# Kernel tuning notes

Measured on AMD Instinct MI355X. Metric: run time of the kernel, lower is better.

## Reference

```python
import jax, jax.numpy as jnp
import numpy as np

N, E, G, F_IN, H, C = 50000, 800000, 512, 128, 96, 10
BN_EPS = 1e-5


def _bn(x, w, b):
    # torch BatchNorm1d training-mode forward: batch stats, biased variance
    mu = jnp.mean(x, axis=0)
    var = jnp.var(x, axis=0)
    return (x - mu) * jax.lax.rsqrt(var + BN_EPS) * w + b


def setup_inputs() -> dict:
    key = jax.random.key(0)
    ks = iter(jax.random.split(key, 64))

    def rn(shape, s=0.05):
        return jax.random.normal(next(ks), shape, jnp.float32) * s

    inp = {
        "x": jax.random.normal(next(ks), (N, F_IN), jnp.float32),
        "edge_index": jax.random.randint(next(ks), (2, E), 0, N, dtype=jnp.int32),
        "batch": jnp.sort(jax.random.randint(next(ks), (N,), 0, G, dtype=jnp.int32)),
        "bn_feat_w": jnp.ones((F_IN,), jnp.float32),
        "bn_feat_b": jnp.full((F_IN,), 1e-4, jnp.float32),
        "Wf": rn((F_IN, H)), "bf": jnp.zeros((H,), jnp.float32),
        "bn_fc_w": jnp.ones((H,), jnp.float32),
        "bn_fc_b": jnp.full((H,), 1e-4, jnp.float32),
        "Wl": rn((H, H)), "bl": jnp.zeros((H,), jnp.float32),
        "bn_hid_w": jnp.ones((H,), jnp.float32),
        "bn_hid_b": jnp.full((H,), 1e-4, jnp.float32),
        "Wc": rn((H, C)), "bc": jnp.zeros((C,), jnp.float32),
    }
    for i in range(3):
        inp[f"W1_{i}"] = rn((H, H)); inp[f"b1_{i}"] = jnp.zeros((H,), jnp.float32)
        inp[f"bnw_{i}"] = jnp.ones((H,), jnp.float32)
        inp[f"bnb_{i}"] = jnp.full((H,), 1e-4, jnp.float32)
        inp[f"W2_{i}"] = rn((H, H)); inp[f"b2_{i}"] = jnp.zeros((H,), jnp.float32)
    return inp


def reference(x, edge_index, batch, bn_feat_w, bn_feat_b, Wf, bf,
              W1_0, b1_0, bnw_0, bnb_0, W2_0, b2_0,
              W1_1, b1_1, bnw_1, bnb_1, W2_1, b2_1,
              W1_2, b1_2, bnw_2, bnb_2, W2_2, b2_2,
              bn_fc_w, bn_fc_b, Wl, bl, bn_hid_w, bn_hid_b, Wc, bc):
    src, dst = edge_index[0], edge_index[1]
    h = _bn(x, bn_feat_w, bn_feat_b)
    # GCNConv(gfn=True): pure linear feature transform, no propagation
    h = jax.nn.relu(h @ Wf + bf)
    gin_params = [
        (W1_0, b1_0, bnw_0, bnb_0, W2_0, b2_0),
        (W1_1, b1_1, bnw_1, bnb_1, W2_1, b2_1),
        (W1_2, b1_2, bnw_2, bnb_2, W2_2, b2_2),
    ]
    for W1, b1, bw, bb, W2, b2 in gin_params:
        # GIN: (1+eps)*x + sum-aggregate of neighbor features (eps=0)
        agg = jax.ops.segment_sum(h[src], dst, num_segments=N)  # [N, H]
        m = h + agg
        m = jax.nn.relu(_bn(m @ W1 + b1, bw, bb))
        h = jax.nn.relu(m @ W2 + b2)
    # global_add_pool over graphs
    g = jax.ops.segment_sum(h, batch, num_segments=G)  # [G, H]
    g = jax.nn.relu(_bn(g, bn_fc_w, bn_fc_b) @ Wl + bl)
    g = _bn(g, bn_hid_w, bn_hid_b)
    logits = g @ Wc + bc
    return jax.nn.log_softmax(logits, axis=-1)
```

## Files before the change

kernel.cpp:

```cpp
#include <hip/hip_runtime.h>

#define N_NODES 50000
#define N_EDGES 800000
#define N_GRAPHS 512
#define F_IN 128
#define HDIM 96
#define NCLS 10
#define BN_EPS 1e-5f

#define NPB 128
#define NBUCK2 ((N_NODES + NPB - 1) / NPB)
#define NEB 128
#define EPB ((N_EDGES + NEB - 1) / NEB)

typedef unsigned int u32;
typedef unsigned short u16;
typedef __attribute__((ext_vector_type(8))) short bf16x8;
typedef __attribute__((ext_vector_type(4))) float f32x4;

__device__ __forceinline__ u16 f2bf(float f) {
    u32 u = __float_as_uint(f);
    u32 r = (u + 0x7fffu + ((u >> 16) & 1u)) >> 16;
    return (u16)r;
}
__device__ __forceinline__ float bflo(u32 w) { return __uint_as_float(w << 16); }
__device__ __forceinline__ float bfhi(u32 w) { return __uint_as_float(w & 0xffff0000u); }

template<int NC>
__global__ __launch_bounds__(256) void colstats4_kernel(const float* __restrict__ in,
                                                        float* __restrict__ stats,
                                                        int nrows) {
    constexpr int CG  = NC / 4;
    constexpr int RPB = 256 / CG;
    const int cg = threadIdx.x % CG;
    const int rg = threadIdx.x / CG;
    float4 s = make_float4(0.f, 0.f, 0.f, 0.f);
    float4 q = make_float4(0.f, 0.f, 0.f, 0.f);
    for (int r = blockIdx.x * RPB + rg; r < nrows; r += gridDim.x * RPB) {
        float4 v = *(const float4*)&in[(size_t)r * NC + cg * 4];
        s.x += v.x; s.y += v.y; s.z += v.z; s.w += v.w;
        q.x += v.x * v.x; q.y += v.y * v.y; q.z += v.z * v.z; q.w += v.w * v.w;
    }
    __shared__ float ss[RPB][NC], sq[RPB][NC];
    *(float4*)&ss[rg][cg * 4] = s;
    *(float4*)&sq[rg][cg * 4] = q;
    __syncthreads();
    if (threadIdx.x < NC) {
        float a = 0.f, b = 0.f;
        #pragma unroll
        for (int r = 0; r < RPB; r++) { a += ss[r][threadIdx.x]; b += sq[r][threadIdx.x]; }
        atomicAdd(&stats[threadIdx.x],      a);
        atomicAdd(&stats[NC + threadIdx.x], b);
    }
}

template<int NC>
__global__ __launch_bounds__(2*NC) void colstats_kernel(const float* __restrict__ in,
                                                        float* __restrict__ stats,
                                                        int nrows) {
    const int col  = threadIdx.x % NC;
    const int half = threadIdx.x / NC;
    float s = 0.f, ss = 0.f;
    for (int r = blockIdx.x * 2 + half; r < nrows; r += gridDim.x * 2) {
        float v = in[(size_t)r * NC + col];
        s += v; ss += v * v;
    }
    __shared__ float shs[2][NC], shq[2][NC];
    shs[half][col] = s; shq[half][col] = ss;
    __syncthreads();
    if (half == 0) {
        atomicAdd(&stats[col],      s  + shs[1][col]);
        atomicAdd(&stats[NC + col], ss + shq[1][col]);
    }
}

__global__ void finalize_bn_kernel(const float* __restrict__ stats,
                                   const float* __restrict__ w,
                                   const float* __restrict__ b,
                                   float* __restrict__ ac, int ncols, float inv_n) {
    int k = blockIdx.x * blockDim.x + threadIdx.x;
    if (k < ncols) {
        float mu  = stats[k] * inv_n;
        float var = stats[ncols + k] * inv_n - mu * mu;
        float a   = w[k] * rsqrtf(var + BN_EPS);
        ac[k]         = a;
        ac[ncols + k] = b[k] - mu * a;
    }
}

template<int KDIM, bool FOLD>
__global__ __launch_bounds__(256) void wprep_kernel(const float* __restrict__ W,
                                                    const float* __restrict__ bias,
                                                    const float* __restrict__ ac,
                                                    u16* __restrict__ wtb,
                                                    float* __restrict__ bmod) {
    int i = blockIdx.x * 256 + threadIdx.x;
    if (i < KDIM * 96) {
        int k = i / 96, n = i % 96;
        float v = W[i];
        if constexpr (FOLD) v *= ac[k];
        wtb[n * KDIM + k] = f2bf(v);
    }
    if (blockIdx.x == 0 && threadIdx.x < 96) {
        float b = bias[threadIdx.x];
        if constexpr (FOLD) {
            for (int k = 0; k < KDIM; k++) b += ac[KDIM + k] * W[k * 96 + threadIdx.x];
        }
        bmod[threadIdx.x] = b;
    }
}

__global__ void hist_kernel(const int* __restrict__ dst, int* __restrict__ deg, int ne) {
    int e = blockIdx.x * blockDim.x + threadIdx.x;
    if (e < ne) atomicAdd(&deg[dst[e]], 1);
}

__global__ __launch_bounds__(1024) void scan1_kernel(const int* __restrict__ in,
                                                     int* __restrict__ tmp,
                                                     int* __restrict__ partial, int n) {
    __shared__ int sh[1024];
    const int i = blockIdx.x * 1024 + threadIdx.x;
    const int d = (i < n) ? in[i] : 0;
    sh[threadIdx.x] = d;
    __syncthreads();
    for (int off = 1; off < 1024; off <<= 1) {
        int v = 0;
        if (threadIdx.x >= off) v = sh[threadIdx.x - off];
        __syncthreads();
        sh[threadIdx.x] += v;
        __syncthreads();
    }
    if (i < n) tmp[i] = sh[threadIdx.x] - d;
    if (threadIdx.x == 1023) partial[blockIdx.x] = sh[1023];
}

__global__ void scan2_kernel(int* __restrict__ partial, int nparts) {
    const int t = threadIdx.x;
    int d = (t < nparts) ? partial[t] : 0;
    int v = d;
    for (int off = 1; off < 64; off <<= 1) {
        int u = __shfl_up(v, off, 64);
        if (t >= off) v += u;
    }
    if (t < nparts) partial[t] = v - d;
}

__global__ __launch_bounds__(1024) void scan3_rowptr_kernel(const int* __restrict__ tmp,
                                                            const int* __restrict__ partial,
                                                            const int* __restrict__ deg,
                                                            int* __restrict__ row_ptr, int n) {
    const int i = blockIdx.x * 1024 + threadIdx.x;
    if (i < n) {
        int v = tmp[i] + partial[blockIdx.x];
        row_ptr[i] = v;
        if (i == n - 1) row_ptr[n] = v + deg[i];
    }
}

__global__ __launch_bounds__(1024) void scan3_kernel(const int* __restrict__ tmp,
                                                     const int* __restrict__ partial,
                                                     int* __restrict__ out, int n) {
    const int i = blockIdx.x * 1024 + threadIdx.x;
    if (i < n) out[i] = tmp[i] + partial[blockIdx.x];
}

__global__ __launch_bounds__(256) void count_kernel(const int* __restrict__ dst,
                                                    int* __restrict__ cnt ) {
    __shared__ int lc[NBUCK2];
    for (int i = threadIdx.x; i < NBUCK2; i += 256) lc[i] = 0;
    __syncthreads();
    const int lo = blockIdx.x * EPB;
    const int hi = min(lo + EPB, N_EDGES);
    for (int e = lo + threadIdx.x; e < hi; e += 256)
        atomicAdd(&lc[dst[e] / NPB], 1);
    __syncthreads();
    for (int i = threadIdx.x; i < NBUCK2; i += 256)
        cnt[i * NEB + blockIdx.x] = lc[i];
}

__global__ __launch_bounds__(256) void distribute_kernel(const int* __restrict__ src,
                                                         const int* __restrict__ dst,
                                                         const int* __restrict__ ofs,
                                                         uint2* __restrict__ ebuf) {
    __shared__ int lofs[NBUCK2];
    for (int i = threadIdx.x; i < NBUCK2; i += 256) lofs[i] = ofs[i * NEB + blockIdx.x];
    __syncthreads();
    const int lo = blockIdx.x * EPB;
    const int hi = min(lo + EPB, N_EDGES);
    for (int e = lo + threadIdx.x; e < hi; e += 256) {
        int d = dst[e];
        int q = atomicAdd(&lofs[d / NPB], 1);
        ebuf[q] = make_uint2((u32)src[e], (u32)d);
    }
}

__global__ __launch_bounds__(256) void bucket_fill_kernel(const uint2* __restrict__ ebuf,
                                                          const int* __restrict__ ofs,
                                                          const int* __restrict__ row_ptr,
                                                          int* __restrict__ csr) {
    __shared__ int cur[NPB];
    const int p    = blockIdx.x;
    const int base = p * NPB;
    const int nn   = min(NPB, N_NODES - base);
    for (int i = threadIdx.x; i < nn; i += 256) cur[i] = row_ptr[base + i];
    __syncthreads();
    const int e0 = ofs[p * NEB];
    const int e1 = (p + 1 < NBUCK2) ? ofs[(p + 1) * NEB] : N_EDGES;
    for (int e = e0 + threadIdx.x; e < e1; e += 256) {
        uint2 v = ebuf[e];
        int pos = atomicAdd(&cur[(int)v.y - base], 1);
        csr[pos] = (int)v.x;
    }
}

__global__ __launch_bounds__(192) void agg_kernel(const u16* __restrict__ hb,
                                                  const int* __restrict__ row_ptr,
                                                  const int* __restrict__ csr,
                                                  u16* __restrict__ mb, int n) {
    const int jj   = threadIdx.x % 24;
    const int node = blockIdx.x * 8 + threadIdx.x / 24;
    if (node >= n) return;
    const int p0 = row_ptr[node], p1 = row_ptr[node + 1];
    uint2 sv = *(const uint2*)&hb[(size_t)node * 96 + jj * 4];
    float a0 = bflo(sv.x), a1 = bfhi(sv.x), a2 = bflo(sv.y), a3 = bfhi(sv.y);
    int p = p0;
    for (; p + 8 <= p1; p += 8) {
        int s0 = csr[p],     s1 = csr[p + 1], s2 = csr[p + 2], s3 = csr[p + 3];
        int s4 = csr[p + 4], s5 = csr[p + 5], s6 = csr[p + 6], s7 = csr[p + 7];
        uint2 v0 = *(const uint2*)&hb[(size_t)s0 * 96 + jj * 4];
        uint2 v1 = *(const uint2*)&hb[(size_t)s1 * 96 + jj * 4];
        uint2 v2 = *(const uint2*)&hb[(size_t)s2 * 96 + jj * 4];
        uint2 v3 = *(const uint2*)&hb[(size_t)s3 * 96 + jj * 4];
        uint2 v4 = *(const uint2*)&hb[(size_t)s4 * 96 + jj * 4];
        uint2 v5 = *(const uint2*)&hb[(size_t)s5 * 96 + jj * 4];
        uint2 v6 = *(const uint2*)&hb[(size_t)s6 * 96 + jj * 4];
        uint2 v7 = *(const uint2*)&hb[(size_t)s7 * 96 + jj * 4];
        a0 += ((bflo(v0.x) + bflo(v1.x)) + (bflo(v2.x) + bflo(v3.x)))
            + ((bflo(v4.x) + bflo(v5.x)) + (bflo(v6.x) + bflo(v7.x)));
        a1 += ((bfhi(v0.x) + bfhi(v1.x)) + (bfhi(v2.x) + bfhi(v3.x)))
            + ((bfhi(v4.x) + bfhi(v5.x)) + (bfhi(v6.x) + bfhi(v7.x)));
        a2 += ((bflo(v0.y) + bflo(v1.y)) + (bflo(v2.y) + bflo(v3.y)))
            + ((bflo(v4.y) + bflo(v5.y)) + (bflo(v6.y) + bflo(v7.y)));
        a3 += ((bfhi(v0.y) + bfhi(v1.y)) + (bfhi(v2.y) + bfhi(v3.y)))
            + ((bfhi(v4.y) + bfhi(v5.y)) + (bfhi(v6.y) + bfhi(v7.y)));
    }
    for (; p < p1; p++) {
        int s = csr[p];
        uint2 v = *(const uint2*)&hb[(size_t)s * 96 + jj * 4];
        a0 += bflo(v.x); a1 += bfhi(v.x); a2 += bflo(v.y); a3 += bfhi(v.y);
    }
    ushort4 o; o.x = f2bf(a0); o.y = f2bf(a1); o.z = f2bf(a2); o.w = f2bf(a3);
    *(ushort4*)&mb[(size_t)node * 96 + jj * 4] = o;
}

template<int KDIM, bool IN_F32, bool IN_AFF_RELU, bool OUT_RELU, bool STATS, bool OUT_BF16, bool POOL>
__global__ __launch_bounds__(256) void mmx_kernel(const void* __restrict__ in_,
                                                  const u16* __restrict__ wt,
                                                  const float* __restrict__ bias,
                                                  const float* __restrict__ ac,
                                                  void* __restrict__ out_,
                                                  float* __restrict__ stats,
                                                  const int* __restrict__ batch,
                                                  int nrows) {
    constexpr int KP = KDIM + 8;
    constexpr int KB = KDIM / 32;
    __shared__ u16 wlds[96 * KP];
    __shared__ u16 alds[64 * KP];
    __shared__ float sred[2][4][96];
    const int tid = threadIdx.x;

    for (int i = tid; i < 96 * (KDIM / 8); i += 256) {
        int nn = i / (KDIM / 8), c8 = i % (KDIM / 8);
        *(uint4*)&wlds[nn * KP + c8 * 8] = *(const uint4*)&wt[nn * KDIM + c8 * 8];
    }

    const int w    = tid >> 6;
    const int lane = tid & 63;
    const int r16  = lane & 15;
    const int kg   = lane >> 4;
    const int m0   = w * 16;
    float bn[6];
    #pragma unroll
    for (int nt = 0; nt < 6; nt++) bn[nt] = bias[nt * 16 + r16];
    float scol[6] = {0,0,0,0,0,0}, qcol[6] = {0,0,0,0,0,0};

    const int nchunks = (nrows + 63) / 64;
    for (int chunk = blockIdx.x; chunk < nchunks; chunk += gridDim.x) {
        const int row0 = chunk * 64;
        __syncthreads();
        if constexpr (IN_F32) {
            const float* inf = (const float*)in_;
            for (int i = tid; i < 64 * (KDIM / 4); i += 256) {
                int r = i / (KDIM / 4), c4 = i % (KDIM / 4);
                int gr = row0 + r;
                float4 v = (gr < nrows) ? *(const float4*)&inf[(size_t)gr * KDIM + c4 * 4]
                                        : make_float4(0.f, 0.f, 0.f, 0.f);
                ushort4 o; o.x = f2bf(v.x); o.y = f2bf(v.y); o.z = f2bf(v.z); o.w = f2bf(v.w);
                *(ushort4*)&alds[r * KP + c4 * 4] = o;
            }
        } else {
            const u16* inb = (const u16*)in_;
            for (int i = tid; i < 64 * (KDIM / 8); i += 256) {
                int r = i / (KDIM / 8), c8 = i % (KDIM / 8);
                int gr = row0 + r;
                uint4 v = (gr < nrows) ? *(const uint4*)&inb[(size_t)gr * KDIM + c8 * 8]
                                       : make_uint4(0u, 0u, 0u, 0u);
                if constexpr (IN_AFF_RELU) {
                    u32 words[4] = {v.x, v.y, v.z, v.w};
                    #pragma unroll
                    for (int t2 = 0; t2 < 4; t2++) {
                        int k0 = c8 * 8 + t2 * 2;
                        float lo = fmaxf(bflo(words[t2]) * ac[k0]     + ac[KDIM + k0],     0.f);
                        float hi = fmaxf(bfhi(words[t2]) * ac[k0 + 1] + ac[KDIM + k0 + 1], 0.f);
                        words[t2] = (u32)f2bf(lo) | ((u32)f2bf(hi) << 16);
                    }
                    v.x = words[0]; v.y = words[1]; v.z = words[2]; v.w = words[3];
                }
                *(uint4*)&alds[r * KP + c8 * 8] = v;
            }
        }
        __syncthreads();

        bf16x8 af[KB];
        #pragma unroll
        for (int kb = 0; kb < KB; kb++)
            af[kb] = *(const bf16x8*)&alds[(m0 + r16) * KP + kb * 32 + kg * 8];

        f32x4 acc[6];
        #pragma unroll
        for (int nt = 0; nt < 6; nt++) acc[nt] = (f32x4){bn[nt], bn[nt], bn[nt], bn[nt]};
        #pragma unroll
        for (int kb = 0; kb < KB; kb++) {
            #pragma unroll
            for (int nt = 0; nt < 6; nt++) {
                bf16x8 bfr = *(const bf16x8*)&wlds[(nt * 16 + r16) * KP + kb * 32 + kg * 8];
                acc[nt] = __builtin_amdgcn_mfma_f32_16x16x32_bf16(af[kb], bfr, acc[nt], 0, 0, 0);
            }
        }

        const int gr0  = row0 + m0 + kg * 4;
        const bool full = (gr0 + 3 < nrows);
        if constexpr (POOL) {
            float* gbuf = (float*)out_;
            int bl = -1, bh = -2;
            if (full) { bl = batch[gr0]; bh = batch[gr0 + 3]; }
            #pragma unroll
            for (int nt = 0; nt < 6; nt++) {
                float v0 = acc[nt][0], v1 = acc[nt][1], v2 = acc[nt][2], v3 = acc[nt][3];
                if constexpr (OUT_RELU) {
                    v0 = fmaxf(v0, 0.f); v1 = fmaxf(v1, 0.f);
                    v2 = fmaxf(v2, 0.f); v3 = fmaxf(v3, 0.f);
                }
                const int n = nt * 16 + r16;
                if (full) {
                    if (bl == bh) {
                        atomicAdd(&gbuf[(size_t)bl * 96 + n], (v0 + v1) + (v2 + v3));
                    } else {
                        atomicAdd(&gbuf[(size_t)batch[gr0]     * 96 + n], v0);
                        atomicAdd(&gbuf[(size_t)batch[gr0 + 1] * 96 + n], v1);
                        atomicAdd(&gbuf[(size_t)batch[gr0 + 2] * 96 + n], v2);
                        atomicAdd(&gbuf[(size_t)batch[gr0 + 3] * 96 + n], v3);
                    }
                } else {
                    if (gr0     < nrows) atomicAdd(&gbuf[(size_t)batch[gr0]     * 96 + n], v0);
                    if (gr0 + 1 < nrows) atomicAdd(&gbuf[(size_t)batch[gr0 + 1] * 96 + n], v1);
                    if (gr0 + 2 < nrows) atomicAdd(&gbuf[(size_t)batch[gr0 + 2] * 96 + n], v2);
                }
            }
        } else {
            #pragma unroll
            for (int nt = 0; nt < 6; nt++) {
                float v[4] = {acc[nt][0], acc[nt][1], acc[nt][2], acc[nt][3]};
                if constexpr (OUT_RELU) {
                    #pragma unroll
                    for (int rr = 0; rr < 4; rr++) v[rr] = fmaxf(v[rr], 0.f);
                }
                const int n = nt * 16 + r16;
                #pragma unroll
                for (int rr = 0; rr < 4; rr++) {
                    const int gr = gr0 + rr;
                    if (full || gr < nrows) {
                        if constexpr (OUT_BF16) ((u16*)out_)[(size_t)gr * 96 + n] = f2bf(v[rr]);
                        else                    ((float*)out_)[(size_t)gr * 96 + n] = v[rr];
                        if constexpr (STATS) { scol[nt] += v[rr]; qcol[nt] += v[rr] * v[rr]; }
                    }
                }
            }
        }
    }

    if constexpr (STATS) {
        #pragma unroll
        for (int nt = 0; nt < 6; nt++) {
            scol[nt] += __shfl_xor(scol[nt], 16);
            scol[nt] += __shfl_xor(scol[nt], 32);
            qcol[nt] += __shfl_xor(qcol[nt], 16);
            qcol[nt] += __shfl_xor(qcol[nt], 32);
        }
        __syncthreads();
        if (kg == 0) {
            #pragma unroll
            for (int nt = 0; nt < 6; nt++) {
                sred[0][w][nt * 16 + r16] = scol[nt];
                sred[1][w][nt * 16 + r16] = qcol[nt];
            }
        }
        __syncthreads();
        if (tid < 96) {
            float a = sred[0][0][tid] + sred[0][1][tid] + sred[0][2][tid] + sred[0][3][tid];
            float b = sred[1][0][tid] + sred[1][1][tid] + sred[1][2][tid] + sred[1][3][tid];
            atomicAdd(&stats[tid],      a);
            atomicAdd(&stats[96 + tid], b);
        }
    }
}

template<int KDIM, bool IN_AFF, bool IN_RELU, bool OUT_RELU, bool STATS>
__global__ __launch_bounds__(192) void mm_kernel(const float* __restrict__ in,
                                                 const float* __restrict__ W,
                                                 const float* __restrict__ bias,
                                                 const float* __restrict__ ac,
                                                 float* __restrict__ out,
                                                 float* __restrict__ stats, int nrows) {
    constexpr int KG = KDIM / 4;
    __shared__ float ws[KDIM][96];
    __shared__ float xs[32][KDIM];
    const int tid = threadIdx.x;
    const int cg  = tid % 24;
    const int rg  = tid / 24;
    for (int i = tid; i < KDIM * 24; i += 192) {
        int k = i / 24, c4 = i % 24;
        *(float4*)&ws[k][c4 * 4] = *(const float4*)&W[(size_t)k * 96 + c4 * 4];
    }
    const float4 bj = *(const float4*)&bias[cg * 4];
    float s0=0,s1=0,s2=0,s3=0, q0=0,q1=0,q2=0,q3=0;
    const int nchunks = (nrows + 31) / 32;
    for (int chunk = blockIdx.x; chunk < nchunks; chunk += gridDim.x) {
        const int row0 = chunk * 32;
        __syncthreads();
        for (int i = tid; i < 32 * KG; i += 192) {
            int r = i / KG, g = i % KG;
            int gr = row0 + r;
            float4 v = make_float4(0.f, 0.f, 0.f, 0.f);
            if (gr < nrows) v = *(const float4*)&in[(size_t)gr * KDIM + g * 4];
            if constexpr (IN_AFF) {
                float4 a = *(const float4*)&ac[g * 4];
                float4 c = *(const float4*)&ac[KDIM + g * 4];
                v.x = v.x * a.x + c.x; v.y = v.y * a.y + c.y;
                v.z = v.z * a.z + c.z; v.w = v.w * a.w + c.w;
            }
            if constexpr (IN_RELU) {
                v.x = fmaxf(v.x, 0.f); v.y = fmaxf(v.y, 0.f);
                v.z = fmaxf(v.z, 0.f); v.w = fmaxf(v.w, 0.f);
            }
            *(float4*)&xs[r][4 * (g ^ (r & 7))] = v;
        }
        __syncthreads();
        float acc[4][4];
        #pragma unroll
        for (int m = 0; m < 4; m++) {
            acc[m][0] = bj.x; acc[m][1] = bj.y; acc[m][2] = bj.z; acc[m][3] = bj.w;
        }
        #pragma unroll 4
        for (int g = 0; g < KG; g++) {
            const int xi = 4 * (g ^ rg);
            float4 xv0 = *(const float4*)&xs[rg     ][xi];
            float4 xv1 = *(const float4*)&xs[rg +  8][xi];
            float4 xv2 = *(const float4*)&xs[rg + 16][xi];
            float4 xv3 = *(const float4*)&xs[rg + 24][xi];
            #pragma unroll
            for (int i = 0; i < 4; i++) {
                float4 wv = *(const float4*)&ws[g * 4 + i][cg * 4];
                float x0 = (i==0)?xv0.x:(i==1)?xv0.y:(i==2)?xv0.z:xv0.w;
                float x1 = (i==0)?xv1.x:(i==1)?xv1.y:(i==2)?xv1.z:xv1.w;
                float x2 = (i==0)?xv2.x:(i==1)?xv2.y:(i==2)?xv2.z:xv2.w;
                float x3 = (i==0)?xv3.x:(i==1)?xv3.y:(i==2)?xv3.z:xv3.w;
                acc[0][0] = fmaf(x0, wv.x, acc[0][0]); acc[0][1] = fmaf(x0, wv.y, acc[0][1]);
                acc[0][2] = fmaf(x0, wv.z, acc[0][2]); acc[0][3] = fmaf(x0, wv.w, acc[0][3]);
                acc[1][0] = fmaf(x1, wv.x, acc[1][0]); acc[1][1] = fmaf(x1, wv.y, acc[1][1]);
                acc[1][2] = fmaf(x1, wv.z, acc[1][2]); acc[1][3] = fmaf(x1, wv.w, acc[1][3]);
                acc[2][0] = fmaf(x2, wv.x, acc[2][0]); acc[2][1] = fmaf(x2, wv.y, acc[2][1]);
                acc[2][2] = fmaf(x2, wv.z, acc[2][2]); acc[2][3] = fmaf(x2, wv.w, acc[2][3]);
                acc[3][0] = fmaf(x3, wv.x, acc[3][0]); acc[3][1] = fmaf(x3, wv.y, acc[3][1]);
                acc[3][2] = fmaf(x3, wv.z, acc[3][2]); acc[3][3] = fmaf(x3, wv.w, acc[3][3]);
            }
        }
        #pragma unroll
        for (int m = 0; m < 4; m++) {
            const int gr = row0 + rg + 8 * m;
            if (gr < nrows) {
                float4 o = make_float4(acc[m][0], acc[m][1], acc[m][2], acc[m][3]);
                if constexpr (OUT_RELU) {
                    o.x = fmaxf(o.x, 0.f); o.y = fmaxf(o.y, 0.f);
                    o.z = fmaxf(o.z, 0.f); o.w = fmaxf(o.w, 0.f);
                }
                *(float4*)&out[(size_t)gr * 96 + cg * 4] = o;
                if constexpr (STATS) {
                    s0 += o.x; q0 += o.x * o.x; s1 += o.y; q1 += o.y * o.y;
                    s2 += o.z; q2 += o.z * o.z; s3 += o.w; q3 += o.w * o.w;
                }
            }
        }
    }
    if constexpr (STATS) {
        __syncthreads();
        float* rs = &xs[0][0];
        float* rq = rs + 8 * 96;
        rs[rg * 96 + cg * 4 + 0] = s0; rs[rg * 96 + cg * 4 + 1] = s1;
        rs[rg * 96 + cg * 4 + 2] = s2; rs[rg * 96 + cg * 4 + 3] = s3;
        rq[rg * 96 + cg * 4 + 0] = q0; rq[rg * 96 + cg * 4 + 1] = q1;
        rq[rg * 96 + cg * 4 + 2] = q2; rq[rg * 96 + cg * 4 + 3] = q3;
        __syncthreads();
        if (tid < 96) {
            float a = 0.f, b = 0.f;
            #pragma unroll
            for (int r = 0; r < 8; r++) { a += rs[r * 96 + tid]; b += rq[r * 96 + tid]; }
            atomicAdd(&stats[tid],      a);
            atomicAdd(&stats[96 + tid], b);
        }
    }
}

__global__ void head_kernel(const float* __restrict__ g1, const float* __restrict__ ac,
                            const float* __restrict__ Wc, const float* __restrict__ bc,
                            float* __restrict__ out, int ngraphs) {
    int gi = blockIdx.x * blockDim.x + threadIdx.x;
    if (gi >= ngraphs) return;
    float v[NCLS];
    #pragma unroll
    for (int c = 0; c < NCLS; c++) v[c] = bc[c];
    for (int k = 0; k < HDIM; k++) {
        float x = g1[(size_t)gi * HDIM + k] * ac[k] + ac[HDIM + k];
        #pragma unroll
        for (int c = 0; c < NCLS; c++) v[c] = fmaf(x, Wc[k * NCLS + c], v[c]);
    }
    float mx = v[0];
    #pragma unroll
    for (int c = 1; c < NCLS; c++) mx = fmaxf(mx, v[c]);
    float sum = 0.f;
    #pragma unroll
    for (int c = 0; c < NCLS; c++) sum += expf(v[c] - mx);
    float lse = mx + logf(sum);
    #pragma unroll
    for (int c = 0; c < NCLS; c++) out[(size_t)gi * NCLS + c] = v[c] - lse;
}

extern "C" void kernel_launch(void* const* d_in, const int* in_sizes, int n_in,
                              void* d_out, int out_size, void* d_ws, size_t ws_size,
                              hipStream_t stream) {
    const float* x         = (const float*)d_in[0];
    const int*   ei        = (const int*)  d_in[1];
    const int*   batch     = (const int*)  d_in[2];
    const float* bn_feat_w = (const float*)d_in[3];
    const float* bn_feat_b = (const float*)d_in[4];
    const float* Wf        = (const float*)d_in[5];
    const float* bfv       = (const float*)d_in[6];
    const float* bn_fc_w   = (const float*)d_in[7];
    const float* bn_fc_b   = (const float*)d_in[8];
    const float* Wl        = (const float*)d_in[9];
    const float* bl        = (const float*)d_in[10];
    const float* bn_hid_w  = (const float*)d_in[11];
    const float* bn_hid_b  = (const float*)d_in[12];
    const float* Wc        = (const float*)d_in[13];
    const float* bc        = (const float*)d_in[14];
    float* out = (float*)d_out;

    char* p = (char*)d_ws;
    auto alloc = [&](size_t bytes) { char* q = p; p += (bytes + 255) & ~(size_t)255; return q; };
    u16*   hb     = (u16*)  alloc((size_t)N_NODES * HDIM * 2);
    u16*   mb     = (u16*)  alloc((size_t)N_NODES * HDIM * 2);
    float* g      = (float*)alloc((size_t)N_GRAPHS * HDIM * 4);
    float* g1     = (float*)alloc((size_t)N_GRAPHS * HDIM * 4);
    float* statsX = (float*)alloc(2 * F_IN * 4);
    float* acX    = (float*)alloc(2 * F_IN * 4);
    float* statsT = (float*)alloc(2 * HDIM * 4);
    float* acT    = (float*)alloc(2 * HDIM * 4);
    float* statsG = (float*)alloc(2 * HDIM * 4);
    float* acG    = (float*)alloc(2 * HDIM * 4);
    float* statsG1= (float*)alloc(2 * HDIM * 4);
    float* acHid  = (float*)alloc(2 * HDIM * 4);
    u16*   wtF    = (u16*)  alloc(96 * F_IN * 2);
    float* bFmod  = (float*)alloc(96 * 4);
    u16*   wt1[3]; u16* wt2[3]; float* b1mod[3]; float* b2mod[3];
    for (int l = 0; l < 3; l++) {
        wt1[l] = (u16*)alloc(96 * HDIM * 2); b1mod[l] = (float*)alloc(96 * 4);
        wt2[l] = (u16*)alloc(96 * HDIM * 2); b2mod[l] = (float*)alloc(96 * 4);
    }
    int* deg      = (int*)alloc((size_t)N_NODES * 4);
    int* row_ptr  = (int*)alloc((size_t)(N_NODES + 1) * 4);
    int* csr      = (int*)alloc((size_t)N_EDGES * 4);
    int* stmp     = (int*)alloc((size_t)N_NODES * 4);
    int* spart    = (int*)alloc(64 * 4);
    int* cnt      = (int*)alloc((size_t)NBUCK2 * NEB * 4);
    int* ofs      = (int*)alloc((size_t)NBUCK2 * NEB * 4);
    int* stmp2    = (int*)alloc((size_t)NBUCK2 * NEB * 4);
    int* spart2   = (int*)alloc(64 * 4);
    uint2* ebuf   = (uint2*)alloc((size_t)N_EDGES * 8);

    const int* srcp = ei;
    const int* dstp = ei + N_EDGES;

    const int nch64  = (N_NODES + 63) / 64;
    const int gridF  = (nch64 < 768) ? nch64 : 768;
    const int grid96 = (nch64 < 1024) ? nch64 : 1024;
    const int gridG  = (N_GRAPHS + 31) / 32;
    const int nscan  = (N_NODES + 1023) / 1024;
    const int ncb    = NBUCK2 * NEB;
    const int nscan2 = (ncb + 1023) / 1024;

    hipMemsetAsync(statsX, 0, 2 * F_IN * 4, stream);
    colstats4_kernel<F_IN><<<256, 256, 0, stream>>>(x, statsX, N_NODES);
    finalize_bn_kernel<<<1, F_IN, 0, stream>>>(statsX, bn_feat_w, bn_feat_b, acX, F_IN, 1.0f / N_NODES);
    wprep_kernel<F_IN, true><<<(F_IN * 96 + 255) / 256, 256, 0, stream>>>(Wf, bfv, acX, wtF, bFmod);
    mmx_kernel<F_IN, true, false, true, false, true, false><<<gridF, 256, 0, stream>>>(x, wtF, bFmod, nullptr, hb, nullptr, nullptr, N_NODES);

    for (int l = 0; l < 3; l++) {
        wprep_kernel<HDIM, false><<<(HDIM * 96 + 255) / 256, 256, 0, stream>>>((const float*)d_in[15 + 6 * l], (const float*)d_in[16 + 6 * l], nullptr, wt1[l], b1mod[l]);
        wprep_kernel<HDIM, false><<<(HDIM * 96 + 255) / 256, 256, 0, stream>>>((const float*)d_in[19 + 6 * l], (const float*)d_in[20 + 6 * l], nullptr, wt2[l], b2mod[l]);
    }

    hipMemsetAsync(deg, 0, (size_t)N_NODES * 4, stream);
    hist_kernel<<<(N_EDGES + 255) / 256, 256, 0, stream>>>(dstp, deg, N_EDGES);
    scan1_kernel<<<nscan, 1024, 0, stream>>>(deg, stmp, spart, N_NODES);
    scan2_kernel<<<1, 64, 0, stream>>>(spart, nscan);
    scan3_rowptr_kernel<<<nscan, 1024, 0, stream>>>(stmp, spart, deg, row_ptr, N_NODES);
    count_kernel<<<NEB, 256, 0, stream>>>(dstp, cnt);
    scan1_kernel<<<nscan2, 1024, 0, stream>>>(cnt, stmp2, spart2, ncb);
    scan2_kernel<<<1, 64, 0, stream>>>(spart2, nscan2);
    scan3_kernel<<<nscan2, 1024, 0, stream>>>(stmp2, spart2, ofs, ncb);
    distribute_kernel<<<NEB, 256, 0, stream>>>(srcp, dstp, ofs, ebuf);
    bucket_fill_kernel<<<NBUCK2, 256, 0, stream>>>(ebuf, ofs, row_ptr, csr);

    hipMemsetAsync(g, 0, (size_t)N_GRAPHS * HDIM * 4, stream);

    for (int l = 0; l < 3; l++) {
        const float* bw = (const float*)d_in[17 + 6 * l];
        const float* bb = (const float*)d_in[18 + 6 * l];
        agg_kernel<<<(N_NODES + 7) / 8, 192, 0, stream>>>(hb, row_ptr, csr, mb, N_NODES);
        hipMemsetAsync(statsT, 0, 2 * HDIM * 4, stream);
        mmx_kernel<HDIM, false, false, false, true, true, false><<<grid96, 256, 0, stream>>>(mb, wt1[l], b1mod[l], nullptr, mb, statsT, nullptr, N_NODES);
        finalize_bn_kernel<<<1, HDIM, 0, stream>>>(statsT, bw, bb, acT, HDIM, 1.0f / N_NODES);
        if (l < 2) {
            mmx_kernel<HDIM, false, true, true, false, true, false><<<grid96, 256, 0, stream>>>(mb, wt2[l], b2mod[l], acT, hb, nullptr, nullptr, N_NODES);
        } else {
            mmx_kernel<HDIM, false, true, true, false, false, true><<<grid96, 256, 0, stream>>>(mb, wt2[l], b2mod[l], acT, g, nullptr, batch, N_NODES);
        }
    }

    hipMemsetAsync(statsG, 0, 2 * HDIM * 4, stream);
    colstats_kernel<HDIM><<<64, 2 * HDIM, 0, stream>>>(g, statsG, N_GRAPHS);
    finalize_bn_kernel<<<1, HDIM, 0, stream>>>(statsG, bn_fc_w, bn_fc_b, acG, HDIM, 1.0f / N_GRAPHS);
    hipMemsetAsync(statsG1, 0, 2 * HDIM * 4, stream);
    mm_kernel<HDIM, true, false, true, true><<<gridG, 192, 0, stream>>>(g, Wl, bl, acG, g1, statsG1, N_GRAPHS);
    finalize_bn_kernel<<<1, HDIM, 0, stream>>>(statsG1, bn_hid_w, bn_hid_b, acHid, HDIM, 1.0f / N_GRAPHS);

    head_kernel<<<2, 256, 0, stream>>>(g1, acHid, Wc, bc, out, N_GRAPHS);
}
```

Before: 389.2 us.

## Fuse degree histogram into bucket count, pack edge buffer, widen aggregation loads

```diff
diff --git a/kernel.cpp b/kernel.cpp
--- a/kernel.cpp
+++ b/kernel.cpp
@@ -110,11 +110,6 @@
     }
 }
 
-__global__ void hist_kernel(const int* __restrict__ dst, int* __restrict__ deg, int ne) {
-    int e = blockIdx.x * blockDim.x + threadIdx.x;
-    if (e < ne) atomicAdd(&deg[dst[e]], 1);
-}
-
 __global__ __launch_bounds__(1024) void scan1_kernel(const int* __restrict__ in,
                                                      int* __restrict__ tmp,
                                                      int* __restrict__ partial, int n) {
@@ -165,14 +160,18 @@
 }
 
 __global__ __launch_bounds__(256) void count_kernel(const int* __restrict__ dst,
+                                                    int* __restrict__ deg,
                                                     int* __restrict__ cnt ) {
     __shared__ int lc[NBUCK2];
     for (int i = threadIdx.x; i < NBUCK2; i += 256) lc[i] = 0;
     __syncthreads();
     const int lo = blockIdx.x * EPB;
     const int hi = min(lo + EPB, N_EDGES);
-    for (int e = lo + threadIdx.x; e < hi; e += 256)
-        atomicAdd(&lc[dst[e] / NPB], 1);
+    for (int e = lo + threadIdx.x; e < hi; e += 256) {
+        int d = dst[e];
+        atomicAdd(&lc[d / NPB], 1);
+        atomicAdd(&deg[d], 1);
+    }
     __syncthreads();
     for (int i = threadIdx.x; i < NBUCK2; i += 256)
         cnt[i * NEB + blockIdx.x] = lc[i];
@@ -181,7 +180,7 @@
 __global__ __launch_bounds__(256) void distribute_kernel(const int* __restrict__ src,
                                                          const int* __restrict__ dst,
                                                          const int* __restrict__ ofs,
-                                                         uint2* __restrict__ ebuf) {
+                                                         u32* __restrict__ ebuf) {
     __shared__ int lofs[NBUCK2];
     for (int i = threadIdx.x; i < NBUCK2; i += 256) lofs[i] = ofs[i * NEB + blockIdx.x];
     __syncthreads();
@@ -190,11 +189,11 @@
     for (int e = lo + threadIdx.x; e < hi; e += 256) {
         int d = dst[e];
         int q = atomicAdd(&lofs[d / NPB], 1);
-        ebuf[q] = make_uint2((u32)src[e], (u32)d);
-    }
-}
-
-__global__ __launch_bounds__(256) void bucket_fill_kernel(const uint2* __restrict__ ebuf,
+        ebuf[q] = ((u32)src[e] << 7) | (u32)(d & (NPB - 1));
+    }
+}
+
+__global__ __launch_bounds__(256) void bucket_fill_kernel(const u32* __restrict__ ebuf,
                                                           const int* __restrict__ ofs,
                                                           const int* __restrict__ row_ptr,
                                                           int* __restrict__ csr) {
@@ -207,9 +206,9 @@
     const int e0 = ofs[p * NEB];
     const int e1 = (p + 1 < NBUCK2) ? ofs[(p + 1) * NEB] : N_EDGES;
     for (int e = e0 + threadIdx.x; e < e1; e += 256) {
-        uint2 v = ebuf[e];
-        int pos = atomicAdd(&cur[(int)v.y - base], 1);
-        csr[pos] = (int)v.x;
+        u32 v = ebuf[e];
+        int pos = atomicAdd(&cur[v & (NPB - 1)], 1);
+        csr[pos] = (int)(v >> 7);
     }
 }
 
@@ -217,24 +216,25 @@
                                                   const int* __restrict__ row_ptr,
                                                   const int* __restrict__ csr,
                                                   u16* __restrict__ mb, int n) {
-    const int jj   = threadIdx.x % 24;
-    const int node = blockIdx.x * 8 + threadIdx.x / 24;
+    const int jj   = threadIdx.x % 12;
+    const int node = blockIdx.x * 16 + threadIdx.x / 12;
     if (node >= n) return;
     const int p0 = row_ptr[node], p1 = row_ptr[node + 1];
-    uint2 sv = *(const uint2*)&hb[(size_t)node * 96 + jj * 4];
+    uint4 sv = *(const uint4*)&hb[(size_t)node * 96 + jj * 8];
     float a0 = bflo(sv.x), a1 = bfhi(sv.x), a2 = bflo(sv.y), a3 = bfhi(sv.y);
+    float a4 = bflo(sv.z), a5 = bfhi(sv.z), a6 = bflo(sv.w), a7 = bfhi(sv.w);
     int p = p0;
     for (; p + 8 <= p1; p += 8) {
         int s0 = csr[p],     s1 = csr[p + 1], s2 = csr[p + 2], s3 = csr[p + 3];
         int s4 = csr[p + 4], s5 = csr[p + 5], s6 = csr[p + 6], s7 = csr[p + 7];
-        uint2 v0 = *(const uint2*)&hb[(size_t)s0 * 96 + jj * 4];
-        uint2 v1 = *(const uint2*)&hb[(size_t)s1 * 96 + jj * 4];
-        uint2 v2 = *(const uint2*)&hb[(size_t)s2 * 96 + jj * 4];
-        uint2 v3 = *(const uint2*)&hb[(size_t)s3 * 96 + jj * 4];
-        uint2 v4 = *(const uint2*)&hb[(size_t)s4 * 96 + jj * 4];
-        uint2 v5 = *(const uint2*)&hb[(size_t)s5 * 96 + jj * 4];
-        uint2 v6 = *(const uint2*)&hb[(size_t)s6 * 96 + jj * 4];
-        uint2 v7 = *(const uint2*)&hb[(size_t)s7 * 96 + jj * 4];
+        uint4 v0 = *(const uint4*)&hb[(size_t)s0 * 96 + jj * 8];
+        uint4 v1 = *(const uint4*)&hb[(size_t)s1 * 96 + jj * 8];
+        uint4 v2 = *(const uint4*)&hb[(size_t)s2 * 96 + jj * 8];
+        uint4 v3 = *(const uint4*)&hb[(size_t)s3 * 96 + jj * 8];
+        uint4 v4 = *(const uint4*)&hb[(size_t)s4 * 96 + jj * 8];
+        uint4 v5 = *(const uint4*)&hb[(size_t)s5 * 96 + jj * 8];
+        uint4 v6 = *(const uint4*)&hb[(size_t)s6 * 96 + jj * 8];
+        uint4 v7 = *(const uint4*)&hb[(size_t)s7 * 96 + jj * 8];
         a0 += ((bflo(v0.x) + bflo(v1.x)) + (bflo(v2.x) + bflo(v3.x)))
             + ((bflo(v4.x) + bflo(v5.x)) + (bflo(v6.x) + bflo(v7.x)));
         a1 += ((bfhi(v0.x) + bfhi(v1.x)) + (bfhi(v2.x) + bfhi(v3.x)))
@@ -243,14 +243,42 @@
             + ((bflo(v4.y) + bflo(v5.y)) + (bflo(v6.y) + bflo(v7.y)));
         a3 += ((bfhi(v0.y) + bfhi(v1.y)) + (bfhi(v2.y) + bfhi(v3.y)))
             + ((bfhi(v4.y) + bfhi(v5.y)) + (bfhi(v6.y) + bfhi(v7.y)));
+        a4 += ((bflo(v0.z) + bflo(v1.z)) + (bflo(v2.z) + bflo(v3.z)))
+            + ((bflo(v4.z) + bflo(v5.z)) + (bflo(v6.z) + bflo(v7.z)));
+        a5 += ((bfhi(v0.z) + bfhi(v1.z)) + (bfhi(v2.z) + bfhi(v3.z)))
+            + ((bfhi(v4.z) + bfhi(v5.z)) + (bfhi(v6.z) + bfhi(v7.z)));
+        a6 += ((bflo(v0.w) + bflo(v1.w)) + (bflo(v2.w) + bflo(v3.w)))
+            + ((bflo(v4.w) + bflo(v5.w)) + (bflo(v6.w) + bflo(v7.w)));
+        a7 += ((bfhi(v0.w) + bfhi(v1.w)) + (bfhi(v2.w) + bfhi(v3.w)))
+            + ((bfhi(v4.w) + bfhi(v5.w)) + (bfhi(v6.w) + bfhi(v7.w)));
+    }
+    for (; p + 4 <= p1; p += 4) {
+        int s0 = csr[p], s1 = csr[p + 1], s2 = csr[p + 2], s3 = csr[p + 3];
+        uint4 v0 = *(const uint4*)&hb[(size_t)s0 * 96 + jj * 8];
+        uint4 v1 = *(const uint4*)&hb[(size_t)s1 * 96 + jj * 8];
+        uint4 v2 = *(const uint4*)&hb[(size_t)s2 * 96 + jj * 8];
+        uint4 v3 = *(const uint4*)&hb[(size_t)s3 * 96 + jj * 8];
+        a0 += (bflo(v0.x) + bflo(v1.x)) + (bflo(v2.x) + bflo(v3.x));
+        a1 += (bfhi(v0.x) + bfhi(v1.x)) + (bfhi(v2.x) + bfhi(v3.x));
+        a2 += (bflo(v0.y) + bflo(v1.y)) + (bflo(v2.y) + bflo(v3.y));
+        a3 += (bfhi(v0.y) + bfhi(v1.y)) + (bfhi(v2.y) + bfhi(v3.y));
+        a4 += (bflo(v0.z) + bflo(v1.z)) + (bflo(v2.z) + bflo(v3.z));
+        a5 += (bfhi(v0.z) + bfhi(v1.z)) + (bfhi(v2.z) + bfhi(v3.z));
+        a6 += (bflo(v0.w) + bflo(v1.w)) + (bflo(v2.w) + bflo(v3.w));
+        a7 += (bfhi(v0.w) + bfhi(v1.w)) + (bfhi(v2.w) + bfhi(v3.w));
     }
     for (; p < p1; p++) {
         int s = csr[p];
-        uint2 v = *(const uint2*)&hb[(size_t)s * 96 + jj * 4];
+        uint4 v = *(const uint4*)&hb[(size_t)s * 96 + jj * 8];
         a0 += bflo(v.x); a1 += bfhi(v.x); a2 += bflo(v.y); a3 += bfhi(v.y);
-    }
-    ushort4 o; o.x = f2bf(a0); o.y = f2bf(a1); o.z = f2bf(a2); o.w = f2bf(a3);
-    *(ushort4*)&mb[(size_t)node * 96 + jj * 4] = o;
+        a4 += bflo(v.z); a5 += bfhi(v.z); a6 += bflo(v.w); a7 += bfhi(v.w);
+    }
+    uint4 o;
+    o.x = (u32)f2bf(a0) | ((u32)f2bf(a1) << 16);
+    o.y = (u32)f2bf(a2) | ((u32)f2bf(a3) << 16);
+    o.z = (u32)f2bf(a4) | ((u32)f2bf(a5) << 16);
+    o.w = (u32)f2bf(a6) | ((u32)f2bf(a7) << 16);
+    *(uint4*)&mb[(size_t)node * 96 + jj * 8] = o;
 }
 
 template<int KDIM, bool IN_F32, bool IN_AFF_RELU, bool OUT_RELU, bool STATS, bool OUT_BF16, bool POOL>
@@ -595,7 +623,7 @@
     int* ofs      = (int*)alloc((size_t)NBUCK2 * NEB * 4);
     int* stmp2    = (int*)alloc((size_t)NBUCK2 * NEB * 4);
     int* spart2   = (int*)alloc(64 * 4);
-    uint2* ebuf   = (uint2*)alloc((size_t)N_EDGES * 8);
+    u32* ebuf     = (u32*)alloc((size_t)N_EDGES * 4);
 
     const int* srcp = ei;
     const int* dstp = ei + N_EDGES;
@@ -620,11 +648,10 @@
     }
 
     hipMemsetAsync(deg, 0, (size_t)N_NODES * 4, stream);
-    hist_kernel<<<(N_EDGES + 255) / 256, 256, 0, stream>>>(dstp, deg, N_EDGES);
+    count_kernel<<<NEB, 256, 0, stream>>>(dstp, deg, cnt);
     scan1_kernel<<<nscan, 1024, 0, stream>>>(deg, stmp, spart, N_NODES);
     scan2_kernel<<<1, 64, 0, stream>>>(spart, nscan);
     scan3_rowptr_kernel<<<nscan, 1024, 0, stream>>>(stmp, spart, deg, row_ptr, N_NODES);
-    count_kernel<<<NEB, 256, 0, stream>>>(dstp, cnt);
     scan1_kernel<<<nscan2, 1024, 0, stream>>>(cnt, stmp2, spart2, ncb);
     scan2_kernel<<<1, 64, 0, stream>>>(spart2, nscan2);
     scan3_kernel<<<nscan2, 1024, 0, stream>>>(stmp2, spart2, ofs, ncb);
@@ -636,7 +663,7 @@
     for (int l = 0; l < 3; l++) {
         const float* bw = (const float*)d_in[17 + 6 * l];
         const float* bb = (const float*)d_in[18 + 6 * l];
-        agg_kernel<<<(N_NODES + 7) / 8, 192, 0, stream>>>(hb, row_ptr, csr, mb, N_NODES);
+        agg_kernel<<<(N_NODES + 15) / 16, 192, 0, stream>>>(hb, row_ptr, csr, mb, N_NODES);
         hipMemsetAsync(statsT, 0, 2 * HDIM * 4, stream);
         mmx_kernel<HDIM, false, false, false, true, true, false><<<grid96, 256, 0, stream>>>(mb, wt1[l], b1mod[l], nullptr, mb, statsT, nullptr, N_NODES);
         finalize_bn_kernel<<<1, HDIM, 0, stream>>>(statsT, bw, bb, acT, HDIM, 1.0f / N_NODES);
```

Measured after the change: 371.5 us. 4.5% less time.
